# Optimization experiments

Hardware: AMD Instinct MI355X
Metric: run time of the kernel (lower is better)

Reference implementation:

```python
import jax, jax.numpy as jnp
import numpy as np

IDIM = 80
ODIM = 80
HDIM = 512
THINK_ITER = 5
TEMPER = 0.7
IGNORE_OUT = 0.0


def pad_for_shift(key, pad, window):
    # key: (B,T,C) -> (B,T,S,window), S = C + 2*pad - window + 1 shifted windows
    C = key.shape[-1]
    kp = jnp.pad(key, ((0, 0), (0, 0), (pad, pad)))
    S = C + 2 * pad - window + 1
    idx = jnp.arange(S)[:, None] + jnp.arange(window)[None, :]  # (S, window)
    return kp[..., idx]


def reverse_pad_for_shift(key, pad, theta):
    # inverse of pad_for_shift selection: out[..., j] = key_pad[..., 2*pad - theta + j]
    C = key.shape[-1]
    kp = jnp.pad(key, ((0, 0), (0, 0), (pad, pad)))
    idx = (2 * pad - theta)[..., None] + jnp.arange(C)  # (B,T,C)
    return jnp.take_along_axis(kp, idx, axis=-1)


def selector(x_aug, y):
    # cosine similarity across shifts; x_aug (B,T,S,c), y (B,T,c)
    dot = jnp.einsum('btsc,btc->bts', x_aug, y)
    denom = jnp.linalg.norm(x_aug, axis=-1) * jnp.linalg.norm(y, axis=-1)[..., None]
    sim = jnp.where(denom == 0, 0.0, dot / jnp.where(denom == 0, 1.0, denom))
    theta = jnp.argmax(sim, axis=-1)                                   # (B,T)
    sim_max = jnp.take_along_axis(sim, theta[..., None], axis=-1)[..., 0]
    y_align = jnp.take_along_axis(x_aug, theta[..., None, None], axis=-2)[..., 0, :]
    return y_align, sim_max, theta


def inference_src(x, W_enc, b_enc, W_src, b_src):
    # conv1d-style matching-pursuit inference, decoder_type='src'
    x_aug = pad_for_shift(x, IDIM, 2 * IDIM)                 # (B,T,IDIM+1,2*IDIM)
    h = jnp.einsum('btsc,hc->btsh', x_aug, W_enc) + b_enc    # (B,T,S,HDIM)
    energy = jnp.sum(h * h, axis=-1)                         # (B,T,S)
    h_ind = jnp.argmax(energy, axis=-1)                      # (B,T)
    h_sel = jnp.take_along_axis(h, h_ind[..., None, None], axis=-2)[..., 0, :]
    x_ext = jnp.einsum('bth,oh->bto', h_sel, W_src) + b_src  # (B,T,2*ODIM)
    # gather contiguous window of length IDIM starting at IDIM - h_ind
    idx = (IDIM - h_ind)[..., None] + jnp.arange(IDIM)       # (B,T,IDIM)
    return jnp.take_along_axis(x_ext, idx, axis=-1)


def seq_loss(pred, target, mask):
    keep = jnp.logical_not(mask)
    sq = jnp.square(pred - target) * keep
    return jnp.sum(sq) / jnp.maximum(jnp.sum(keep), 1)


def _forward(x, y, W_enc, b_enc, W_src, b_src):
    seq_mask = (y == IGNORE_OUT)
    y_res, x_res = y, x
    losses = []
    for _ in range(THINK_ITER):
        x_aug = pad_for_shift(x_res, ODIM - 1, ODIM)         # (B,T,2*ODIM-1,ODIM)
        y_align, sim_opt, theta = selector(x_aug, y_res)
        attn = jax.nn.softmax(y_align * y_res / TEMPER, axis=-1)
        y_att = y_align * attn
        x_ele = reverse_pad_for_shift(y_att, ODIM - 1, theta)
        y_ele = inference_src(y_att, W_enc, b_enc, W_src, b_src)
        losses.append(seq_loss(y_ele, y_res, seq_mask))
        y_res = jax.lax.stop_gradient(y_res - y_ele)
        x_res = jax.lax.stop_gradient(x_res - x_ele)
    return jnp.mean(jnp.stack(losses))


def setup_inputs():
    key = jax.random.key(0)
    ks = jax.random.split(key, 6)
    B, T = 4, 256
    x = jax.random.normal(ks[0], (B, T, IDIM), dtype=jnp.float32)
    y = jax.random.normal(ks[1], (B, T, ODIM), dtype=jnp.float32)
    s_e = 1.0 / np.sqrt(2 * IDIM)
    s_d = 1.0 / np.sqrt(HDIM)
    W_enc = jax.random.uniform(ks[2], (HDIM, 2 * IDIM), jnp.float32, -s_e, s_e)
    b_enc = jax.random.uniform(ks[3], (HDIM,), jnp.float32, -s_e, s_e)
    W_src = jax.random.uniform(ks[4], (2 * ODIM, HDIM), jnp.float32, -s_d, s_d)
    b_src = jax.random.uniform(ks[5], (2 * ODIM,), jnp.float32, -s_d, s_d)
    return {"x": x, "y": y, "W_enc": W_enc, "b_enc": b_enc, "W_src": W_src, "b_src": b_src}


def reference(x, y, W_enc, b_enc, W_src, b_src):
    return _forward(x, y, W_enc, b_enc, W_src, b_src)
```

## Files before the change

### kernel.cpp

```cpp
#include <hip/hip_runtime.h>

#define WS_XRES   0
#define WS_YRES   81920
#define WS_WT     163840
#define WS_MT     245760
#define WS_D0     271360
#define WS_G      327680
#define WS_U      353920
#define WS_BB     354080
#define WS_K      354081
#define WS_LOSS   354082
#define WS_YA     354088
#define WS_XELE   444200
#define WS_EN     526120
#define WS_YAT    612160

#define GPITCH 164

__device__ __forceinline__ float rl(float v, int l) {
    return __int_as_float(__builtin_amdgcn_readlane(__float_as_int(v), l));
}

__global__ void k_init(const float* __restrict__ x, const float* __restrict__ y,
                       const float* __restrict__ Wenc, float* __restrict__ ws) {
    int i = blockIdx.x * 256 + threadIdx.x;
    ws[WS_XRES + i] = x[i];
    ws[WS_YRES + i] = y[i];
    int f = i / 160, c = i - f * 160;
    ws[WS_WT + c * 512 + f] = Wenc[i];
    if (i == 0) {
        ws[WS_K] = 0.0f;
        for (int t = 0; t < 5; ++t) ws[WS_LOSS + t] = 0.0f;
    }
}

__device__ __forceinline__ float wave_sum(float v) {
    for (int d = 32; d > 0; d >>= 1) v += __shfl_down(v, d);
    return __shfl(v, 0);
}
__device__ __forceinline__ float wave_max(float v) {
    for (int d = 32; d > 0; d >>= 1) v = fmaxf(v, __shfl_down(v, d));
    return __shfl(v, 0);
}
__device__ __forceinline__ int wave_argmax(float v, int i) {
    for (int d = 32; d > 0; d >>= 1) {
        float v2 = __shfl_down(v, d);
        int   i2 = __shfl_down(i, d);
        if (v2 > v || (v2 == v && i2 < i)) { v = v2; i = i2; }
    }
    return __shfl(i, 0);
}

__global__ __launch_bounds__(256)
void k_cnt(const float* __restrict__ y, float* __restrict__ ws) {
    __shared__ int red[256];
    int tid = threadIdx.x;
    int i = blockIdx.x * 256 + tid;
    red[tid] = (y[i] != 0.0f) ? 1 : 0;
    __syncthreads();
    for (int s = 128; s > 0; s >>= 1) {
        if (tid < s) red[tid] += red[tid + s];
        __syncthreads();
    }
    if (tid == 0) atomicAdd(&ws[WS_K], (float)red[0]);
}

__global__ __launch_bounds__(256)
void k_pre(const float* __restrict__ Wenc, const float* __restrict__ benc,
           float* __restrict__ ws) {
    const int b = blockIdx.x, tid = threadIdx.x;
    __shared__ float wr[512];
    if (b < 160) {
        wr[tid] = ws[WS_WT + b * 512 + tid];
        wr[tid + 256] = ws[WS_WT + b * 512 + 256 + tid];
        __syncthreads();
        if (tid < 160) {
            const float* Wc = Wenc + tid;
            float a0 = 0.f, a1 = 0.f, a2 = 0.f, a3 = 0.f;
            for (int f = 0; f < 512; f += 4) {
                a0 = fmaf(wr[f],     Wc[f * 160],       a0);
                a1 = fmaf(wr[f + 1], Wc[(f + 1) * 160], a1);
                a2 = fmaf(wr[f + 2], Wc[(f + 2) * 160], a2);
                a3 = fmaf(wr[f + 3], Wc[(f + 3) * 160], a3);
            }
            ws[WS_G + b * GPITCH + tid] = (a0 + a1) + (a2 + a3);
        }
    } else {
        wr[tid] = benc[tid];
        wr[tid + 256] = benc[tid + 256];
        __syncthreads();
        if (tid < 160) {
            const float* Wc = Wenc + tid;
            float a0 = 0.f, a1 = 0.f, a2 = 0.f, a3 = 0.f;
            for (int f = 0; f < 512; f += 4) {
                a0 = fmaf(wr[f],     Wc[f * 160],       a0);
                a1 = fmaf(wr[f + 1], Wc[(f + 1) * 160], a1);
                a2 = fmaf(wr[f + 2], Wc[(f + 2) * 160], a2);
                a3 = fmaf(wr[f + 3], Wc[(f + 3) * 160], a3);
            }
            ws[WS_U + tid] = (a0 + a1) + (a2 + a3);
        }
        if (tid < 64) {
            float a = 0.0f;
#pragma unroll
            for (int jj = 0; jj < 8; ++jj) {
                float bv = wr[tid + 64 * jj];
                a = fmaf(bv, bv, a);
            }
            a = wave_sum(a);
            if (tid == 0) ws[WS_BB] = a;
        }
    }
}

__global__ __launch_bounds__(256)
void k_preM(const float* __restrict__ Wenc, const float* __restrict__ benc,
            const float* __restrict__ Wsrc, float* __restrict__ ws) {
    const int o = blockIdx.x, tid = threadIdx.x;
    __shared__ float wr[512];
    wr[tid] = Wsrc[o * 512 + tid];
    wr[tid + 256] = Wsrc[o * 512 + 256 + tid];
    __syncthreads();
    if (tid < 160) {
        const float* Wc = Wenc + tid;
        float a0 = 0.f, a1 = 0.f, a2 = 0.f, a3 = 0.f;
        for (int f = 0; f < 512; f += 4) {
            a0 = fmaf(wr[f],     Wc[f * 160],       a0);
            a1 = fmaf(wr[f + 1], Wc[(f + 1) * 160], a1);
            a2 = fmaf(wr[f + 2], Wc[(f + 2) * 160], a2);
            a3 = fmaf(wr[f + 3], Wc[(f + 3) * 160], a3);
        }
        ws[WS_MT + tid * 160 + o] = (a0 + a1) + (a2 + a3);
    }
    if (tid < 64) {
        float a = 0.0f;
#pragma unroll
        for (int jj = 0; jj < 8; ++jj)
            a = fmaf(wr[tid + 64 * jj], benc[tid + 64 * jj], a);
        a = wave_sum(a);
        if (tid == 0) ws[WS_D0 + o] = a;
    }
}

__global__ __launch_bounds__(128)
void k_sel(float* __restrict__ ws) {
    const int p = blockIdx.x, tid = threadIdx.x, lane = tid & 63;
    const int base = p * 80;
    __shared__ float xr[80], yr[80], simS[160], ya[88];
    __shared__ float s_ny2;

    if (tid < 80) { xr[tid] = ws[WS_XRES + base + tid]; yr[tid] = ws[WS_YRES + base + tid]; }
    __syncthreads();

    if (tid < 64) {
        float a = yr[lane];
        float v = a * a;
        if (lane < 16) { float u = yr[64 + lane]; v = fmaf(u, u, v); }
        v = wave_sum(v);
        if (lane == 0) s_ny2 = v;
    }
    __syncthreads();

    for (int s = tid; s < 159; s += 128) {
        int ilo = (s - 79 > 0) ? s - 79 : 0;
        int ihi = (s < 79) ? s : 79;
        float dot = 0.0f, nx2 = 0.0f;
        for (int i = ilo; i <= ihi; ++i) {
            float xv = xr[i];
            dot = fmaf(xv, yr[i - s + 79], dot);
            nx2 = fmaf(xv, xv, nx2);
        }
        float denom = sqrtf(nx2) * sqrtf(s_ny2);
        simS[s] = (denom == 0.0f) ? 0.0f : dot / denom;
    }
    __syncthreads();

    if (tid < 64) {
        int theta;
        {
            float v = simS[lane]; int i = lane;
            { float v2 = simS[lane + 64]; int i2 = lane + 64;
              if (v2 > v || (v2 == v && i2 < i)) { v = v2; i = i2; } }
            if (lane < 31) {
                float v2 = simS[lane + 128]; int i2 = lane + 128;
                if (v2 > v || (v2 == v && i2 < i)) { v = v2; i = i2; }
            }
            theta = wave_argmax(v, i);
        }
        int t0 = lane, t1 = lane + 64;
        int ix0 = theta + t0 - 79;
        float ya0 = (ix0 >= 0 && ix0 < 80) ? xr[ix0] : 0.0f;
        float z0 = ya0 * yr[t0] / 0.7f;
        float ya1 = 0.0f, z1 = -INFINITY;
        if (t1 < 80) {
            int ix1 = theta + t1 - 79;
            ya1 = (ix1 >= 0 && ix1 < 80) ? xr[ix1] : 0.0f;
            z1 = ya1 * yr[t1] / 0.7f;
        }
        float m = wave_max(fmaxf(z0, z1));
        float e0 = expf(z0 - m);
        float e1 = (t1 < 80) ? expf(z1 - m) : 0.0f;
        float S = wave_sum(e0 + e1);
        float v0 = ya0 * (e0 / S);
        ya[t0] = v0;
        ws[WS_YA + p * 88 + t0] = v0;
        ws[WS_YAT + t0 * 1024 + p] = v0;
        if (t1 < 80) {
            float v1 = ya1 * (e1 / S);
            ya[t1] = v1;
            ws[WS_YA + p * 88 + t1] = v1;
            ws[WS_YAT + t1 * 1024 + p] = v1;
        }
        if (lane < 8) ws[WS_YA + p * 88 + 80 + lane] = 0.0f;
        int k0 = 79 - theta + t0;
        ws[WS_XELE + base + t0] = (k0 >= 0 && k0 < 80) ? ya[k0] : 0.0f;
        if (t1 < 80) {
            int k1 = 79 - theta + t1;
            ws[WS_XELE + base + t1] = (k1 >= 0 && k1 < 80) ? ya[k1] : 0.0f;
        }
    }
}

__global__ __launch_bounds__(256, 4)
void k_conv(const float* __restrict__ G, const float* __restrict__ uvec,
            const float* __restrict__ yat, const float* __restrict__ bbp,
            float* __restrict__ en) {
    const int bid = blockIdx.x;
    const int s   = bid >> 4;
    const int pg  = bid & 15;
    const int c0  = 80 - s;
    const int tid = threadIdx.x;
    const int pl  = tid & 63;
    const int wv  = tid >> 6;
    const int p   = pg * 64 + pl;

    __shared__ float e_l[256];

    float yreg[80];
#pragma unroll
    for (int t = 0; t < 80; ++t) yreg[t] = yat[t * 1024 + p];
#pragma unroll
    for (int t = 0; t < 80; ++t) asm volatile("" : "+v"(yreg[t]));

    const int r0 = wv * 20;
    const float* Grow = G + (c0 + r0) * GPITCH + c0;
    const float* up = uvec + c0 + r0;

    float gm = Grow[pl];
    float gt = (pl < 16) ? Grow[64 + pl] : 0.0f;
    float e = 0.0f;
#pragma unroll 1
    for (int rr = 0; rr < 20; ++rr) {
        float gm_n = 0.0f, gt_n = 0.0f;
        if (rr < 19) {
            const float* nx = Grow + (rr + 1) * GPITCH;
            gm_n = nx[pl];
            gt_n = (pl < 16) ? nx[64 + pl] : 0.0f;
        }
        float a0 = 0.f, a1 = 0.f, a2 = 0.f, a3 = 0.f;
#pragma unroll
        for (int j = 0; j < 20; ++j) a0 = fmaf(rl(gm, j),      yreg[j],      a0);
#pragma unroll
        for (int j = 0; j < 20; ++j) a1 = fmaf(rl(gm, 20 + j), yreg[20 + j], a1);
#pragma unroll
        for (int j = 0; j < 20; ++j) a2 = fmaf(rl(gm, 40 + j), yreg[40 + j], a2);
#pragma unroll
        for (int j = 0; j < 4; ++j)  a3 = fmaf(rl(gm, 60 + j), yreg[60 + j], a3);
#pragma unroll
        for (int j = 0; j < 16; ++j) a3 = fmaf(rl(gt, j),      yreg[64 + j], a3);
        const float vk = (a0 + a1) + (a2 + a3);
        const float uk = up[rr];
        const float yk = yat[(r0 + rr) * 1024 + p];
        e = fmaf(yk, vk + 2.0f * uk, e);
        gm = gm_n; gt = gt_n;
    }
    e_l[tid] = e;
    __syncthreads();
    if (tid < 64)
        en[(pg * 64 + tid) * 84 + s] = bbp[0] +
            ((e_l[tid] + e_l[tid + 64]) + (e_l[tid + 128] + e_l[tid + 192]));
}

__global__ __launch_bounds__(128)
void k_fuse(const float* __restrict__ yorig, const float* __restrict__ bsrc,
            float* __restrict__ ws, int it) {
    const int p = blockIdx.x, tid = threadIdx.x;
    const int lane = tid & 63;
    const int base = p * 80;

    __shared__ float ya_l[84], yr_l[80], xr_l[80], xele_l[80];
    __shared__ float xext80[80];
    __shared__ float yr2[80], xr2[80], simS[160], ya_n[88];
    __shared__ float s_ny2;
    __shared__ int s_hind;

    if (tid < 84) ya_l[tid] = ws[WS_YA + p * 88 + tid];
    if (tid < 80) {
        yr_l[tid]   = ws[WS_YRES + base + tid];
        xr_l[tid]   = ws[WS_XRES + base + tid];
        xele_l[tid] = ws[WS_XELE + base + tid];
    }
    __syncthreads();

    if (tid < 64) {
        float v = ws[WS_EN + p * 84 + lane]; int i = lane;
        if (lane < 17) {
            float v2 = ws[WS_EN + p * 84 + lane + 64]; int i2 = lane + 64;
            if (v2 > v || (v2 == v && i2 < i)) { v = v2; i = i2; }
        }
        int hind = wave_argmax(v, i);
        if (lane == 0) s_hind = hind;
    }
    __syncthreads();
    const int hd = s_hind;
    const int cb = 80 - hd;

    if (tid < 80) {
        const int o = cb + tid;
        const float* M = ws + WS_MT + cb * 160 + o;
        float a0 = bsrc[o] + ws[WS_D0 + o], a1 = 0.f, a2 = 0.f, a3 = 0.f;
        for (int k = 0; k < 80; k += 4) {
            a0 = fmaf(ya_l[k],     M[k * 160],       a0);
            a1 = fmaf(ya_l[k + 1], M[(k + 1) * 160], a1);
            a2 = fmaf(ya_l[k + 2], M[(k + 2) * 160], a2);
            a3 = fmaf(ya_l[k + 3], M[(k + 3) * 160], a3);
        }
        xext80[tid] = (a0 + a1) + (a2 + a3);
    }
    __syncthreads();

    if (tid < 64) {
        int t0 = lane, t1 = lane + 64;
        float sq;
        {
            float yele = xext80[t0];
            float yv = yr_l[t0];
            float keep = (yorig[base + t0] != 0.0f) ? 1.0f : 0.0f;
            float d = yele - yv;
            sq = d * d * keep;
            float ynew = yv - yele;
            float xnew = xr_l[t0] - xele_l[t0];
            yr2[t0] = ynew; xr2[t0] = xnew;
            ws[WS_YRES + base + t0] = ynew;
            ws[WS_XRES + base + t0] = xnew;
        }
        if (t1 < 80) {
            float yele = xext80[t1];
            float yv = yr_l[t1];
            float keep = (yorig[base + t1] != 0.0f) ? 1.0f : 0.0f;
            float d = yele - yv;
            sq = fmaf(d * keep, d, sq);
            float ynew = yv - yele;
            float xnew = xr_l[t1] - xele_l[t1];
            yr2[t1] = ynew; xr2[t1] = xnew;
            ws[WS_YRES + base + t1] = ynew;
            ws[WS_XRES + base + t1] = xnew;
        }
        sq = wave_sum(sq);
        if (lane == 0) atomicAdd(&ws[WS_LOSS + it], sq);
    }
    if (it == 4) return;
    __syncthreads();

    if (tid < 64) {
        float a = yr2[lane];
        float v = a * a;
        if (lane < 16) { float u = yr2[64 + lane]; v = fmaf(u, u, v); }
        v = wave_sum(v);
        if (lane == 0) s_ny2 = v;
    }
    __syncthreads();

    for (int s = tid; s < 159; s += 128) {
        int ilo = (s - 79 > 0) ? s - 79 : 0;
        int ihi = (s < 79) ? s : 79;
        float dot = 0.0f, nx2 = 0.0f;
        for (int i = ilo; i <= ihi; ++i) {
            float xv = xr2[i];
            dot = fmaf(xv, yr2[i - s + 79], dot);
            nx2 = fmaf(xv, xv, nx2);
        }
        float denom = sqrtf(nx2) * sqrtf(s_ny2);
        simS[s] = (denom == 0.0f) ? 0.0f : dot / denom;
    }
    __syncthreads();

    if (tid < 64) {
        int theta;
        {
            float v = simS[lane]; int i = lane;
            { float v2 = simS[lane + 64]; int i2 = lane + 64;
              if (v2 > v || (v2 == v && i2 < i)) { v = v2; i = i2; } }
            if (lane < 31) {
                float v2 = simS[lane + 128]; int i2 = lane + 128;
                if (v2 > v || (v2 == v && i2 < i)) { v = v2; i = i2; }
            }
            theta = wave_argmax(v, i);
        }
        int t0 = lane, t1 = lane + 64;
        int ix0 = theta + t0 - 79;
        float ya0 = (ix0 >= 0 && ix0 < 80) ? xr2[ix0] : 0.0f;
        float z0 = ya0 * yr2[t0] / 0.7f;
        float ya1 = 0.0f, z1 = -INFINITY;
        if (t1 < 80) {
            int ix1 = theta + t1 - 79;
            ya1 = (ix1 >= 0 && ix1 < 80) ? xr2[ix1] : 0.0f;
            z1 = ya1 * yr2[t1] / 0.7f;
        }
        float m = wave_max(fmaxf(z0, z1));
        float e0 = expf(z0 - m);
        float e1 = (t1 < 80) ? expf(z1 - m) : 0.0f;
        float S = wave_sum(e0 + e1);
        float v0 = ya0 * (e0 / S);
        ya_n[t0] = v0;
        ws[WS_YA + p * 88 + t0] = v0;
        ws[WS_YAT + t0 * 1024 + p] = v0;
        if (t1 < 80) {
            float v1 = ya1 * (e1 / S);
            ya_n[t1] = v1;
            ws[WS_YA + p * 88 + t1] = v1;
            ws[WS_YAT + t1 * 1024 + p] = v1;
        }
        if (lane < 8) ws[WS_YA + p * 88 + 80 + lane] = 0.0f;
        int k0 = 79 - theta + t0;
        ws[WS_XELE + base + t0] = (k0 >= 0 && k0 < 80) ? ya_n[k0] : 0.0f;
        if (t1 < 80) {
            int k1 = 79 - theta + t1;
            ws[WS_XELE + base + t1] = (k1 >= 0 && k1 < 80) ? ya_n[k1] : 0.0f;
        }
    }
}

__global__ void k_final(const float* __restrict__ ws, float* __restrict__ out) {
    float K = ws[WS_K];
    if (K < 1.0f) K = 1.0f;
    out[0] = (ws[WS_LOSS] + ws[WS_LOSS + 1] + ws[WS_LOSS + 2] +
              ws[WS_LOSS + 3] + ws[WS_LOSS + 4]) / (K * 5.0f);
}

extern "C" void kernel_launch(void* const* d_in, const int* in_sizes, int n_in,
                              void* d_out, int out_size, void* d_ws, size_t ws_size,
                              hipStream_t stream) {
    const float* x    = (const float*)d_in[0];
    const float* y    = (const float*)d_in[1];
    const float* Wenc = (const float*)d_in[2];
    const float* benc = (const float*)d_in[3];
    const float* Wsrc = (const float*)d_in[4];
    const float* bsrc = (const float*)d_in[5];
    float* ws  = (float*)d_ws;
    float* out = (float*)d_out;

    k_init<<<320, 256, 0, stream>>>(x, y, Wenc, ws);
    k_cnt<<<320, 256, 0, stream>>>(y, ws);
    k_pre<<<161, 256, 0, stream>>>(Wenc, benc, ws);
    k_preM<<<160, 256, 0, stream>>>(Wenc, benc, Wsrc, ws);
    k_sel<<<1024, 128, 0, stream>>>(ws);
    for (int it = 0; it < 5; ++it) {
        k_conv<<<81 * 16, 256, 0, stream>>>(ws + WS_G, ws + WS_U, ws + WS_YAT,
                                            ws + WS_BB, ws + WS_EN);
        k_fuse<<<1024, 128, 0, stream>>>(y, bsrc, ws, it);
    }
    k_final<<<1, 1, 0, stream>>>(ws, out);
}
```

Before: 323.7 us.

## Tile k_conv inner product over column chunks to cut register pressure

```diff
diff --git a/kernel.cpp b/kernel.cpp
--- a/kernel.cpp
+++ b/kernel.cpp
@@ -236,43 +236,37 @@
 
     __shared__ float e_l[256];
 
-    float yreg[80];
-#pragma unroll
-    for (int t = 0; t < 80; ++t) yreg[t] = yat[t * 1024 + p];
-#pragma unroll
-    for (int t = 0; t < 80; ++t) asm volatile("" : "+v"(yreg[t]));
-
     const int r0 = wv * 20;
     const float* Grow = G + (c0 + r0) * GPITCH + c0;
+
+    float acc[20];
+#pragma unroll
+    for (int rr = 0; rr < 20; ++rr) acc[rr] = 0.0f;
+
+#pragma unroll 1
+    for (int jt = 0; jt < 4; ++jt) {
+        float yreg[20];
+#pragma unroll
+        for (int j = 0; j < 20; ++j) yreg[j] = yat[(jt * 20 + j) * 1024 + p];
+#pragma unroll
+        for (int j = 0; j < 20; ++j) asm volatile("" : "+v"(yreg[j]));
+        const float* Gj = Grow + jt * 20;
+#pragma unroll
+        for (int rr = 0; rr < 20; ++rr) {
+            float gm = Gj[rr * GPITCH + pl];
+            float a = acc[rr];
+#pragma unroll
+            for (int j = 0; j < 20; ++j) a = fmaf(rl(gm, j), yreg[j], a);
+            acc[rr] = a;
+        }
+    }
+
     const float* up = uvec + c0 + r0;
-
-    float gm = Grow[pl];
-    float gt = (pl < 16) ? Grow[64 + pl] : 0.0f;
     float e = 0.0f;
-#pragma unroll 1
+#pragma unroll
     for (int rr = 0; rr < 20; ++rr) {
-        float gm_n = 0.0f, gt_n = 0.0f;
-        if (rr < 19) {
-            const float* nx = Grow + (rr + 1) * GPITCH;
-            gm_n = nx[pl];
-            gt_n = (pl < 16) ? nx[64 + pl] : 0.0f;
-        }
-        float a0 = 0.f, a1 = 0.f, a2 = 0.f, a3 = 0.f;
-#pragma unroll
-        for (int j = 0; j < 20; ++j) a0 = fmaf(rl(gm, j),      yreg[j],      a0);
-#pragma unroll
-        for (int j = 0; j < 20; ++j) a1 = fmaf(rl(gm, 20 + j), yreg[20 + j], a1);
-#pragma unroll
-        for (int j = 0; j < 20; ++j) a2 = fmaf(rl(gm, 40 + j), yreg[40 + j], a2);
-#pragma unroll
-        for (int j = 0; j < 4; ++j)  a3 = fmaf(rl(gm, 60 + j), yreg[60 + j], a3);
-#pragma unroll
-        for (int j = 0; j < 16; ++j) a3 = fmaf(rl(gt, j),      yreg[64 + j], a3);
-        const float vk = (a0 + a1) + (a2 + a3);
-        const float uk = up[rr];
-        const float yk = yat[(r0 + rr) * 1024 + p];
-        e = fmaf(yk, vk + 2.0f * uk, e);
-        gm = gm_n; gt = gt_n;
+        float yk = yat[(r0 + rr) * 1024 + p];
+        e = fmaf(yk, acc[rr] + 2.0f * up[rr], e);
     }
     e_l[tid] = e;
     __syncthreads();
```

Measured after the change: 298.6 us. 7.8% less time.
